# Performance work log

Measured on AMD Instinct MI355X. Metric: run time of the kernel, lower is better.

The kernel has to match this reference:

```python
import jax, jax.numpy as jnp
import numpy as np

MAX_BIN = 256
N_SAMPLES = 2_000_000
N_FEATURES = 64


def setup_inputs() -> dict:
    key = jax.random.key(0)
    k1, k2, k3 = jax.random.split(key, 3)
    X = jax.random.randint(k1, (N_SAMPLES, N_FEATURES), 0, MAX_BIN, dtype=jnp.int32)
    gradient = jax.random.normal(k2, (N_SAMPLES,), dtype=jnp.float32)
    hessian = jax.random.uniform(k3, (N_SAMPLES,), dtype=jnp.float32)
    return {"X": X, "gradient": gradient, "hessian": hessian}


def reference(X, gradient, hessian):
    # PGBM split_decision: Gl[f, b] = sum_i gradient[i] * (X[i, f] <= b)
    # Implemented as a per-feature histogram scatter-add, then cumsum over bins.
    def per_feature(xf):  # xf: [N] int bins for one feature
        hg = jax.ops.segment_sum(gradient, xf, num_segments=MAX_BIN)
        hh = jax.ops.segment_sum(hessian, xf, num_segments=MAX_BIN)
        return hg, hh

    hist_g, hist_h = jax.vmap(per_feature, in_axes=1)(X)  # [F, MAX_BIN] each
    Gl = jnp.cumsum(hist_g, axis=1)  # left gradient sums per (feature, bin)
    Hl = jnp.cumsum(hist_h, axis=1)  # left hessian sums per (feature, bin)
    return Gl[None], Hl[None]  # [1, F, MAX_BIN] each, matching unsqueeze(0)
```

## Files before the change

### kernel.cpp

```cpp
#include <hip/hip_runtime.h>

#define N_FEAT 64
#define NBINS 256
#define NB2 260
#define HIST_FLOATS (N_FEAT * NBINS)
#define NBLOCKS 256
#define BLOCK_T 128
#define CHUNK 32
#define PARTIAL_FLOATS (2 * HIST_FLOATS)
#define WS_PARTIAL_BYTES ((size_t)NBLOCKS * PARTIAL_FLOATS * sizeof(float))

__device__ __forceinline__ void load_bins(const int* __restrict__ Xl,
    int c, int rend, int (&bins)[CHUNK])
{
    if (c + CHUNK <= rend) {
        #pragma unroll
        for (int j = 0; j < CHUNK; ++j)
            bins[j] = Xl[(size_t)(c + j) * N_FEAT];
    } else {
        #pragma unroll
        for (int j = 0; j < CHUNK; ++j) {
            int r = c + j; r = r < rend ? r : rend - 1;
            bins[j] = Xl[(size_t)r * N_FEAT];
        }
    }
}

__device__ __forceinline__ void load_vals(const float* __restrict__ vp,
    int c, int rend, float (&val)[CHUNK])
{
    if (c + CHUNK <= rend) {
        #pragma unroll
        for (int j = 0; j < CHUNK / 4; ++j) {
            const float4 v4 = *reinterpret_cast<const float4*>(vp + c + 4 * j);
            val[4*j+0] = v4.x; val[4*j+1] = v4.y; val[4*j+2] = v4.z; val[4*j+3] = v4.w;
        }
    } else {
        #pragma unroll
        for (int j = 0; j < CHUNK; ++j)
            val[j] = (c + j < rend) ? vp[c + j] : 0.f;
    }
}

__device__ __forceinline__ void process_chunk(float* __restrict__ hrow,
    const int (&bins)[CHUNK], const float (&val)[CHUNK])
{
    #pragma unroll
    for (int q = 0; q < CHUNK / 4; ++q) {
        const int   b0 = bins[4*q+0], b1 = bins[4*q+1], b2 = bins[4*q+2], b3 = bins[4*q+3];
        const float v0 = val[4*q+0], v1 = val[4*q+1], v2 = val[4*q+2], v3 = val[4*q+3];
        const bool e10 = b1 == b0;
        const bool e20 = b2 == b0, e21 = b2 == b1;
        const bool e30 = b3 == b0, e31 = b3 == b1, e32 = b3 == b2;
        const float s0 = v0 + (e10 ? v1 : 0.f) + (e20 ? v2 : 0.f) + (e30 ? v3 : 0.f);
        const float s1 = v1 + ((!e20 && e21) ? v2 : 0.f) + ((!e30 && e31) ? v3 : 0.f);
        const float s2 = v2 + ((!e30 && !e31 && e32) ? v3 : 0.f);
        const float s3 = v3;
        const int a0 = b0;
        const int a1 = e10                 ? 256 : b1;
        const int a2 = (e20 || e21)        ? 257 : b2;
        const int a3 = (e30 || e31 || e32) ? 258 : b3;
        const float t0 = hrow[a0], t1 = hrow[a1], t2 = hrow[a2], t3 = hrow[a3];
        hrow[a0] = t0 + s0;
        hrow[a1] = t1 + s1;
        hrow[a2] = t2 + s2;
        hrow[a3] = t3 + s3;
    }
}

__global__ __launch_bounds__(BLOCK_T, 1) void _split_hist_kernel(
    const int* __restrict__ X, const float* __restrict__ grad,
    const float* __restrict__ hess, float* __restrict__ ws, int n, int mode)
{
    __shared__ float hist[2][N_FEAT][NB2];
    const int tid  = threadIdx.x;
    const int w    = tid >> 6;
    const int lane = tid & 63;

    for (int i = tid; i < 2 * N_FEAT * NB2; i += BLOCK_T)
        (&hist[0][0][0])[i] = 0.f;
    __syncthreads();

    const float* vp   = w ? hess : grad;
    const int*   Xl   = X + lane;
    float*       hrow = &hist[w][lane][0];

    const int R    = (((n + NBLOCKS - 1) / NBLOCKS) + CHUNK - 1) / CHUNK * CHUNK;
    const int rbeg = blockIdx.x * R;
    const int rend = min(rbeg + R, n);

    if (rbeg < rend) {
        int   binsA[CHUNK], binsB[CHUNK];
        float valA[CHUNK], valB[CHUNK];
        load_bins(Xl, rbeg, rend, binsA);
        load_vals(vp, rbeg, rend, valA);
        for (int c = rbeg; c < rend; c += 2 * CHUNK) {
            const int c1 = c + CHUNK, c2 = c + 2 * CHUNK;
            if (c1 < rend) {
                load_bins(Xl, c1, rend, binsB);
                load_vals(vp, c1, rend, valB);
            }
            process_chunk(hrow, binsA, valA);
            if (c1 < rend) {
                if (c2 < rend) {
                    load_bins(Xl, c2, rend, binsA);
                    load_vals(vp, c2, rend, valA);
                }
                process_chunk(hrow, binsB, valB);
            }
        }
    }
    __syncthreads();

    if (mode) {
        float* dst = ws + (size_t)blockIdx.x * PARTIAL_FLOATS;
        for (int i = tid; i < PARTIAL_FLOATS; i += BLOCK_T) {
            const int ty  = i >> 14;
            const int fe  = (i >> 8) & 63;
            const int bin = i & 255;
            dst[i] = hist[ty][fe][bin];
        }
    } else {
        for (int i = tid; i < PARTIAL_FLOATS; i += BLOCK_T) {
            const int ty  = i >> 14;
            const int fe  = (i >> 8) & 63;
            const int bin = i & 255;
            unsafeAtomicAdd(&ws[i], hist[ty][fe][bin]);
        }
    }
}

__global__ __launch_bounds__(NBINS) void _split_scan_kernel(
    const float* __restrict__ ws, float* __restrict__ out, int mode)
{
    __shared__ float s[NBINS];
    const int row = blockIdx.x;
    const int t   = threadIdx.x;

    float acc = 0.f;
    if (mode) {
        const size_t slot = (size_t)row * NBINS + t;
        for (int p = 0; p < NBLOCKS; ++p)
            acc += ws[(size_t)p * PARTIAL_FLOATS + slot];
    } else {
        acc = ws[row * NBINS + t];
    }
    s[t] = acc;
    __syncthreads();

    #pragma unroll
    for (int off = 1; off < NBINS; off <<= 1) {
        float x = (t >= off) ? s[t - off] : 0.f;
        __syncthreads();
        s[t] += x;
        __syncthreads();
    }
    out[row * NBINS + t] = s[t];
}

extern "C" void kernel_launch(void* const* d_in, const int* in_sizes, int n_in,
                              void* d_out, int out_size, void* d_ws, size_t ws_size,
                              hipStream_t stream) {
    const int*   X    = (const int*)d_in[0];
    const float* grad = (const float*)d_in[1];
    const float* hess = (const float*)d_in[2];
    float*       out  = (float*)d_out;
    float*       ws   = (float*)d_ws;
    const int n = in_sizes[1];

    const int mode = (ws_size >= WS_PARTIAL_BYTES) ? 1 : 0;
    if (!mode)
        hipMemsetAsync(d_ws, 0, 2 * HIST_FLOATS * sizeof(float), stream);

    hipLaunchKernelGGL(_split_hist_kernel, dim3(NBLOCKS), dim3(BLOCK_T), 0, stream,
                       X, grad, hess, ws, n, mode);
    hipLaunchKernelGGL(_split_scan_kernel, dim3(2 * N_FEAT), dim3(NBINS), 0, stream,
                       ws, out, mode);
}
```

Measured before the change: 942.9 us.

## Split each feature histogram across two waves by bin half, unroll partial reduction

```diff
diff --git a/kernel.cpp b/kernel.cpp
--- a/kernel.cpp
+++ b/kernel.cpp
@@ -2,11 +2,13 @@
 
 #define N_FEAT 64
 #define NBINS 256
-#define NB2 260
+#define LB 128
+#define REGION 133
 #define HIST_FLOATS (N_FEAT * NBINS)
 #define NBLOCKS 256
-#define BLOCK_T 128
+#define BLOCK_T 256
 #define CHUNK 32
+#define NREGION (2 * N_FEAT * 2)
 #define PARTIAL_FLOATS (2 * HIST_FLOATS)
 #define WS_PARTIAL_BYTES ((size_t)NBLOCKS * PARTIAL_FLOATS * sizeof(float))
 
@@ -43,7 +45,7 @@
 }
 
 __device__ __forceinline__ void process_chunk(float* __restrict__ hrow,
-    const int (&bins)[CHUNK], const float (&val)[CHUNK])
+    int halfbit, const int (&bins)[CHUNK], const float (&val)[CHUNK])
 {
     #pragma unroll
     for (int q = 0; q < CHUNK / 4; ++q) {
@@ -56,10 +58,14 @@
         const float s1 = v1 + ((!e20 && e21) ? v2 : 0.f) + ((!e30 && e31) ? v3 : 0.f);
         const float s2 = v2 + ((!e30 && !e31 && e32) ? v3 : 0.f);
         const float s3 = v3;
-        const int a0 = b0;
-        const int a1 = e10                 ? 256 : b1;
-        const int a2 = (e20 || e21)        ? 257 : b2;
-        const int a3 = (e30 || e31 || e32) ? 258 : b3;
+        const bool r0 = (b0 & LB) == halfbit;
+        const bool r1 = ((b1 & LB) == halfbit) && !e10;
+        const bool r2 = ((b2 & LB) == halfbit) && !(e20 || e21);
+        const bool r3 = ((b3 & LB) == halfbit) && !(e30 || e31 || e32);
+        const int a0 = r0 ? (b0 & (LB - 1)) : (LB + 0);
+        const int a1 = r1 ? (b1 & (LB - 1)) : (LB + 1);
+        const int a2 = r2 ? (b2 & (LB - 1)) : (LB + 2);
+        const int a3 = r3 ? (b3 & (LB - 1)) : (LB + 3);
         const float t0 = hrow[a0], t1 = hrow[a1], t2 = hrow[a2], t3 = hrow[a3];
         hrow[a0] = t0 + s0;
         hrow[a1] = t1 + s1;
@@ -72,18 +78,21 @@
     const int* __restrict__ X, const float* __restrict__ grad,
     const float* __restrict__ hess, float* __restrict__ ws, int n, int mode)
 {
-    __shared__ float hist[2][N_FEAT][NB2];
+    __shared__ float hist[NREGION * REGION];
     const int tid  = threadIdx.x;
     const int w    = tid >> 6;
+    const int type = w >> 1;
+    const int half = w & 1;
     const int lane = tid & 63;
 
-    for (int i = tid; i < 2 * N_FEAT * NB2; i += BLOCK_T)
-        (&hist[0][0][0])[i] = 0.f;
+    for (int i = tid; i < NREGION * REGION; i += BLOCK_T)
+        hist[i] = 0.f;
     __syncthreads();
 
-    const float* vp   = w ? hess : grad;
-    const int*   Xl   = X + lane;
-    float*       hrow = &hist[w][lane][0];
+    const float* vp      = type ? hess : grad;
+    const int*   Xl      = X + lane;
+    float*       hrow    = &hist[(((type * N_FEAT + lane) << 1) + half) * REGION];
+    const int    halfbit = half << 7;
 
     const int R    = (((n + NBLOCKS - 1) / NBLOCKS) + CHUNK - 1) / CHUNK * CHUNK;
     const int rbeg = blockIdx.x * R;
@@ -100,13 +109,13 @@
                 load_bins(Xl, c1, rend, binsB);
                 load_vals(vp, c1, rend, valB);
             }
-            process_chunk(hrow, binsA, valA);
+            process_chunk(hrow, halfbit, binsA, valA);
             if (c1 < rend) {
                 if (c2 < rend) {
                     load_bins(Xl, c2, rend, binsA);
                     load_vals(vp, c2, rend, valA);
                 }
-                process_chunk(hrow, binsB, valB);
+                process_chunk(hrow, halfbit, binsB, valB);
             }
         }
     }
@@ -118,14 +127,16 @@
             const int ty  = i >> 14;
             const int fe  = (i >> 8) & 63;
             const int bin = i & 255;
-            dst[i] = hist[ty][fe][bin];
+            const int reg = ((ty * N_FEAT + fe) << 1) + (bin >> 7);
+            dst[i] = hist[reg * REGION + (bin & (LB - 1))];
         }
     } else {
         for (int i = tid; i < PARTIAL_FLOATS; i += BLOCK_T) {
             const int ty  = i >> 14;
             const int fe  = (i >> 8) & 63;
             const int bin = i & 255;
-            unsafeAtomicAdd(&ws[i], hist[ty][fe][bin]);
+            const int reg = ((ty * N_FEAT + fe) << 1) + (bin >> 7);
+            unsafeAtomicAdd(&ws[i], hist[reg * REGION + (bin & (LB - 1))]);
         }
     }
 }
@@ -140,8 +151,15 @@
     float acc = 0.f;
     if (mode) {
         const size_t slot = (size_t)row * NBINS + t;
-        for (int p = 0; p < NBLOCKS; ++p)
-            acc += ws[(size_t)p * PARTIAL_FLOATS + slot];
+        float a0 = 0.f, a1 = 0.f, a2 = 0.f, a3 = 0.f;
+        #pragma unroll 8
+        for (int p = 0; p < NBLOCKS; p += 4) {
+            a0 += ws[(size_t)(p + 0) * PARTIAL_FLOATS + slot];
+            a1 += ws[(size_t)(p + 1) * PARTIAL_FLOATS + slot];
+            a2 += ws[(size_t)(p + 2) * PARTIAL_FLOATS + slot];
+            a3 += ws[(size_t)(p + 3) * PARTIAL_FLOATS + slot];
+        }
+        acc = (a0 + a1) + (a2 + a3);
     } else {
         acc = ws[row * NBINS + t];
     }
```

Result: slower. 1.021 ms (+8.3%).
